# Kernel optimization log

Measured on AMD Instinct MI355X. Metric: run time of the kernel, lower is better.

The kernel has to match this reference:

```python
import jax, jax.numpy as jnp
import numpy as np

B, S, D, H, E, K = 2, 1024, 1024, 2048, 8, 2


def setup_inputs() -> dict:
    key = jax.random.key(0)
    k1, k2, k3, k4 = jax.random.split(key, 4)
    x = jax.random.normal(k1, (B, S, D), dtype=jnp.float32)
    # router initialized to zeros in the module; use small random weights so
    # top-k routing is non-degenerate for a correctness baseline
    router_w = 0.02 * jax.random.normal(k2, (E, D), dtype=jnp.float32)
    router_b = jnp.zeros((E,), dtype=jnp.float32)
    w12 = 0.02 * jax.random.normal(k3, (E, D, 2 * H), dtype=jnp.float32)
    w3 = 0.02 * jax.random.normal(k4, (E, H, D), dtype=jnp.float32)
    return {"x": x, "router_w": router_w, "router_b": router_b, "w12": w12, "w3": w3}


def reference(x, router_w, router_b, w12, w3):
    # Router (eval mode: no jitter noise)
    logits = jnp.einsum("bsd,ed->bse", x, router_w) + router_b      # [B,S,E]
    scores = jax.nn.sigmoid(logits)
    top_vals, top_idx = jax.lax.top_k(scores, K)                     # [B,S,K]
    rweights = top_vals / (jnp.sum(top_vals, axis=-1, keepdims=True) + 1e-6)
    # per-expert combine weight: sum over top-k slots where idx == e
    onehot = jax.nn.one_hot(top_idx, E, dtype=x.dtype)               # [B,S,K,E]
    combine = jnp.einsum("bsk,bske->bse", rweights, onehot)          # [B,S,E]
    # Dense per-expert SwiGLU over all tokens (matches naive module math)
    h12 = jnp.einsum("bsd,edh->ebsh", x, w12)                        # [E,B,S,2H]
    h1, h2 = jnp.split(h12, 2, axis=-1)
    hidden = jax.nn.silu(h1) * h2                                    # [E,B,S,H]
    expert_out = jnp.einsum("ebsh,ehd->ebsd", hidden, w3)            # [E,B,S,D]
    out = jnp.einsum("ebsd,bse->bsd", expert_out, combine)           # [B,S,D]
    aux_loss = 0.01 * jnp.mean(logits ** 2)
    return out, aux_loss
```

## Files before the change

### kernel.cpp

```cpp
#include <hip/hip_runtime.h>
#include <math.h>
#include <stdint.h>

#define B_ 2
#define S_ 1024
#define D_ 1024
#define H_ 2048
#define E_ 8
#define TOK_ (B_*S_)
#define N1_ (2*H_)
#define PAIRS_ (TOK_*2)
#define MAXTILES_ 40

typedef float f32x4 __attribute__((ext_vector_type(4)));
typedef short short8 __attribute__((ext_vector_type(8)));

__device__ __forceinline__ unsigned short f2bf(float f) {
  unsigned int u = __float_as_uint(f);
  u += 0x7fffu + ((u >> 16) & 1u);
  return (unsigned short)(u >> 16);
}

__global__ __launch_bounds__(256) void transpose_f32_to_bf16(
    const float* __restrict__ src, unsigned short* __restrict__ dst, int R, int C)
{
  __shared__ float tile[64][65];
  const int e = blockIdx.z;
  const float* s = src + (size_t)e * R * C;
  unsigned short* d = dst + (size_t)e * R * C;
  const int c0 = blockIdx.x * 64, r0 = blockIdx.y * 64;
  const int tx = threadIdx.x & 63;
  const int ty = threadIdx.x >> 6;
#pragma unroll
  for (int i = 0; i < 16; ++i) {
    int r = ty + i * 4;
    tile[r][tx] = s[(size_t)(r0 + r) * C + c0 + tx];
  }
  __syncthreads();
  const int rx = (threadIdx.x & 31) * 2;
  const int cy = threadIdx.x >> 5;
#pragma unroll
  for (int i = 0; i < 8; ++i) {
    int c = cy + i * 8;
    ushort2 o;
    o.x = f2bf(tile[rx][c]);
    o.y = f2bf(tile[rx + 1][c]);
    *(ushort2*)&d[(size_t)(c0 + c) * R + r0 + rx] = o;
  }
}

__global__ __launch_bounds__(256) void router_kernel(
    const float* __restrict__ x, const float* __restrict__ rw,
    const float* __restrict__ rb, int* __restrict__ counts,
    int* __restrict__ expert_of, int* __restrict__ slot_of,
    float* __restrict__ w_of, float* __restrict__ tok_ssq)
{
  const int wave = threadIdx.x >> 6, lane = threadIdx.x & 63;
  const int t = blockIdx.x * 4 + wave;
  const float4* x4 = (const float4*)(x + (size_t)t * D_);
  const float4* rw4 = (const float4*)rw;
  float acc[E_];
#pragma unroll
  for (int e = 0; e < E_; ++e) acc[e] = 0.f;
#pragma unroll
  for (int d4 = 0; d4 < D_ / 4 / 64; ++d4) {
    int idx = d4 * 64 + lane;
    float4 xv = x4[idx];
#pragma unroll
    for (int e = 0; e < E_; ++e) {
      float4 wv = rw4[e * (D_ / 4) + idx];
      acc[e] += xv.x * wv.x + xv.y * wv.y + xv.z * wv.z + xv.w * wv.w;
    }
  }
#pragma unroll
  for (int e = 0; e < E_; ++e) {
    float v = acc[e];
#pragma unroll
    for (int sh = 32; sh > 0; sh >>= 1) v += __shfl_xor(v, sh, 64);
    acc[e] = v;
  }
  if (lane == 0) {
    float logits[E_], sc[E_], ssq = 0.f;
#pragma unroll
    for (int e = 0; e < E_; ++e) {
      logits[e] = acc[e] + rb[e];
      ssq += logits[e] * logits[e];
      sc[e] = 1.f / (1.f + __expf(-logits[e]));
    }
    tok_ssq[t] = ssq;
    int i1 = 0;
#pragma unroll
    for (int e = 1; e < E_; ++e) if (sc[e] > sc[i1]) i1 = e;
    int i2 = (i1 == 0) ? 1 : 0;
#pragma unroll
    for (int e = 0; e < E_; ++e)
      if (e != i1 && e != i2 && sc[e] > sc[i2]) i2 = e;
    float v1 = sc[i1], v2 = sc[i2];
    float inv = 1.f / (v1 + v2 + 1e-6f);
    int s1 = atomicAdd(&counts[i1], 1);
    int s2 = atomicAdd(&counts[i2], 1);
    expert_of[t * 2]     = i1; slot_of[t * 2]     = s1; w_of[t * 2]     = v1 * inv;
    expert_of[t * 2 + 1] = i2; slot_of[t * 2 + 1] = s2; w_of[t * 2 + 1] = v2 * inv;
  }
}

__global__ __launch_bounds__(256) void meta_kernel(
    const int* __restrict__ counts, const float* __restrict__ tok_ssq,
    int* __restrict__ offsets, int* __restrict__ tile_e, int* __restrict__ tile_m0,
    float* __restrict__ out_aux)
{
  if (threadIdx.x == 0) {
    int o = 0, nt = 0;
    for (int e = 0; e < E_; ++e) {
      offsets[e] = o;
      for (int m0 = 0; m0 < counts[e]; m0 += 128) {
        tile_e[nt] = e; tile_m0[nt] = m0; ++nt;
      }
      o += counts[e];
    }
    for (; nt < MAXTILES_; ++nt) tile_e[nt] = -1;
  }
  __shared__ float sm[256];
  float s = 0.f;
  for (int i = threadIdx.x; i < TOK_; i += 256) s += tok_ssq[i];
  sm[threadIdx.x] = s;
  __syncthreads();
  for (int h = 128; h > 0; h >>= 1) {
    if (threadIdx.x < h) sm[threadIdx.x] += sm[threadIdx.x + h];
    __syncthreads();
  }
  if (threadIdx.x == 0) *out_aux = 0.01f * sm[0] / (float)(TOK_ * E_);
}

__global__ __launch_bounds__(256) void pack_kernel(
    const float* __restrict__ x, const int* __restrict__ expert_of,
    const int* __restrict__ slot_of, const int* __restrict__ offsets,
    unsigned short* __restrict__ px, int* __restrict__ pair_row)
{
  const int pair = blockIdx.x;
  const int t = pair >> 1;
  const int e = expert_of[pair];
  const int row = offsets[e] + slot_of[pair];
  if (threadIdx.x == 0) pair_row[pair] = row;
  const float4* xr = (const float4*)(x + (size_t)t * D_);
  ushort4* pr = (ushort4*)(px + (size_t)row * D_);
  float4 v = xr[threadIdx.x];
  ushort4 o;
  o.x = f2bf(v.x); o.y = f2bf(v.y); o.z = f2bf(v.z); o.w = f2bf(v.w);
  pr[threadIdx.x] = o;
}

__device__ __forceinline__ void stage_tile(const unsigned short* gbase, int gstride,
                                           unsigned short* sbase, int kk,
                                           int wave, int lane)
{
  const int seg = (lane & 3) ^ ((lane >> 3) & 3);
#pragma unroll
  for (int c = 0; c < 2; ++c) {
    const unsigned short* g = gbase
        + (size_t)(wave * 32 + c * 16 + (lane >> 2)) * gstride + kk + seg * 8;
    unsigned short* s = sbase + (wave * 32 + c * 16) * 32;
    __builtin_amdgcn_global_load_lds(
        (const __attribute__((address_space(1))) void*)g,
        (__attribute__((address_space(3))) void*)s, 16, 0, 0);
  }
}

__device__ __forceinline__ void stage_tile_clamped(const unsigned short* gbase, int gstride,
                                                   int row0, int rowmax,
                                                   unsigned short* sbase, int kk,
                                                   int wave, int lane)
{
  const int seg = (lane & 3) ^ ((lane >> 3) & 3);
#pragma unroll
  for (int c = 0; c < 2; ++c) {
    int r = row0 + wave * 32 + c * 16 + (lane >> 2);
    r = (r < rowmax) ? r : rowmax - 1;
    const unsigned short* g = gbase + (size_t)r * gstride + kk + seg * 8;
    unsigned short* s = sbase + (wave * 32 + c * 16) * 32;
    __builtin_amdgcn_global_load_lds(
        (const __attribute__((address_space(1))) void*)g,
        (__attribute__((address_space(3))) void*)s, 16, 0, 0);
  }
}

__device__ __forceinline__ short8 read_frag(const unsigned short* smem, int row, int lk) {
  const int s = lk ^ ((row >> 1) & 3);
  return *(const short8*)&smem[row * 32 + s * 8];
}

__global__ __launch_bounds__(256, 2) void gemm1_kernel(
    const unsigned short* __restrict__ px, const unsigned short* __restrict__ w12t,
    unsigned short* __restrict__ hid, const int* __restrict__ counts,
    const int* __restrict__ offsets, const int* __restrict__ tile_e,
    const int* __restrict__ tile_m0)
{
  const int ti = blockIdx.y, nt = blockIdx.x;
  const int e = tile_e[ti];
  if (e < 0) return;
  const int m0 = tile_m0[ti];
  const int cnt = counts[e];
  const int off = offsets[e];
  const int tid = threadIdx.x;
  const int wave = tid >> 6, lane = tid & 63;
  const int wm = wave >> 1, wn = wave & 1;
  const int lr = lane & 15, lk = lane >> 4;

  __shared__ __align__(16) unsigned short As[128 * 32];
  __shared__ __align__(16) unsigned short B1s[128 * 32];
  __shared__ __align__(16) unsigned short B2s[128 * 32];

  f32x4 zero = {0.f, 0.f, 0.f, 0.f};
  f32x4 acc1[4][4], acc2[4][4];
#pragma unroll
  for (int mi = 0; mi < 4; ++mi)
#pragma unroll
    for (int ni = 0; ni < 4; ++ni) { acc1[mi][ni] = zero; acc2[mi][ni] = zero; }

  const unsigned short* B1base = w12t + ((size_t)e * N1_ + nt * 128) * D_;
  const unsigned short* B2base = w12t + ((size_t)e * N1_ + H_ + nt * 128) * D_;

  for (int kk = 0; kk < D_; kk += 32) {
    stage_tile_clamped(px, D_, off + m0, PAIRS_, As, kk, wave, lane);
    stage_tile(B1base, D_, B1s, kk, wave, lane);
    stage_tile(B2base, D_, B2s, kk, wave, lane);
    __syncthreads();
    short8 a[4], b1[4], b2[4];
#pragma unroll
    for (int i = 0; i < 4; ++i) {
      a[i]  = read_frag(As,  wm * 64 + i * 16 + lr, lk);
      b1[i] = read_frag(B1s, wn * 64 + i * 16 + lr, lk);
      b2[i] = read_frag(B2s, wn * 64 + i * 16 + lr, lk);
    }
#pragma unroll
    for (int mi = 0; mi < 4; ++mi)
#pragma unroll
      for (int ni = 0; ni < 4; ++ni) {
        acc1[mi][ni] = __builtin_amdgcn_mfma_f32_16x16x32_bf16(a[mi], b1[ni], acc1[mi][ni], 0, 0, 0);
        acc2[mi][ni] = __builtin_amdgcn_mfma_f32_16x16x32_bf16(a[mi], b2[ni], acc2[mi][ni], 0, 0, 0);
      }
    __syncthreads();
  }

#pragma unroll
  for (int mi = 0; mi < 4; ++mi)
#pragma unroll
    for (int r = 0; r < 4; ++r) {
      int row_local = m0 + wm * 64 + mi * 16 + lk * 4 + r;
      if (row_local < cnt) {
#pragma unroll
        for (int ni = 0; ni < 4; ++ni) {
          int col = nt * 128 + wn * 64 + ni * 16 + lr;
          float v1 = acc1[mi][ni][r];
          float v2 = acc2[mi][ni][r];
          float hval = (v1 / (1.f + __expf(-v1))) * v2;
          hid[(size_t)(off + row_local) * H_ + col] = f2bf(hval);
        }
      }
    }
}

__global__ __launch_bounds__(256, 4) void gemm2_kernel(
    const unsigned short* __restrict__ hid, const unsigned short* __restrict__ w3t,
    const int* __restrict__ counts, const int* __restrict__ offsets,
    const int* __restrict__ tile_e, const int* __restrict__ tile_m0,
    float* __restrict__ ybuf)
{
  const int ti = blockIdx.y, nt = blockIdx.x, ks = blockIdx.z;
  const int e = tile_e[ti];
  if (e < 0) return;
  const int m0 = tile_m0[ti];
  const int cnt = counts[e];
  const int off = offsets[e];
  const int tid = threadIdx.x;
  const int wave = tid >> 6, lane = tid & 63;
  const int wm = wave >> 1, wn = wave & 1;
  const int lr = lane & 15, lk = lane >> 4;

  __shared__ __align__(16) unsigned short As[128 * 32];
  __shared__ __align__(16) unsigned short Bs[128 * 32];

  f32x4 zero = {0.f, 0.f, 0.f, 0.f};
  f32x4 acc[4][4];
#pragma unroll
  for (int mi = 0; mi < 4; ++mi)
#pragma unroll
    for (int ni = 0; ni < 4; ++ni) acc[mi][ni] = zero;

  const unsigned short* Bbase = w3t + ((size_t)e * D_ + nt * 128) * H_;
  float* yb = ybuf + (size_t)ks * PAIRS_ * D_;

  const int k0 = ks * (H_ / 2), k1 = k0 + (H_ / 2);
  for (int kk = k0; kk < k1; kk += 32) {
    stage_tile_clamped(hid, H_, off + m0, PAIRS_, As, kk, wave, lane);
    stage_tile(Bbase, H_, Bs, kk, wave, lane);
    __syncthreads();
    short8 a[4], b[4];
#pragma unroll
    for (int i = 0; i < 4; ++i) {
      a[i] = read_frag(As, wm * 64 + i * 16 + lr, lk);
      b[i] = read_frag(Bs, wn * 64 + i * 16 + lr, lk);
    }
#pragma unroll
    for (int mi = 0; mi < 4; ++mi)
#pragma unroll
      for (int ni = 0; ni < 4; ++ni)
        acc[mi][ni] = __builtin_amdgcn_mfma_f32_16x16x32_bf16(a[mi], b[ni], acc[mi][ni], 0, 0, 0);
    __syncthreads();
  }

#pragma unroll
  for (int mi = 0; mi < 4; ++mi)
#pragma unroll
    for (int r = 0; r < 4; ++r) {
      int row_local = m0 + wm * 64 + mi * 16 + lk * 4 + r;
      if (row_local < cnt) {
        int g = off + row_local;
#pragma unroll
        for (int ni = 0; ni < 4; ++ni) {
          int col = nt * 128 + wn * 64 + ni * 16 + lr;
          yb[(size_t)g * D_ + col] = acc[mi][ni][r];
        }
      }
    }
}

__global__ __launch_bounds__(256) void combine_kernel(
    const float* __restrict__ ybuf, const int* __restrict__ pair_row,
    const float* __restrict__ w_of, float* __restrict__ out)
{
  const int t = blockIdx.x;
  const int r0 = pair_row[t * 2], r1 = pair_row[t * 2 + 1];
  const float w0 = w_of[t * 2], w1 = w_of[t * 2 + 1];
  const float4* y0 = (const float4*)(ybuf);
  const float4* y1 = (const float4*)(ybuf + (size_t)PAIRS_ * D_);
  const int i = threadIdx.x;
  float4 a0 = y0[(size_t)r0 * (D_ / 4) + i];
  float4 b0 = y1[(size_t)r0 * (D_ / 4) + i];
  float4 a1 = y0[(size_t)r1 * (D_ / 4) + i];
  float4 b1 = y1[(size_t)r1 * (D_ / 4) + i];
  float4 o;
  o.x = w0 * (a0.x + b0.x) + w1 * (a1.x + b1.x);
  o.y = w0 * (a0.y + b0.y) + w1 * (a1.y + b1.y);
  o.z = w0 * (a0.z + b0.z) + w1 * (a1.z + b1.z);
  o.w = w0 * (a0.w + b0.w) + w1 * (a1.w + b1.w);
  ((float4*)out)[(size_t)t * (D_ / 4) + i] = o;
}

extern "C" void kernel_launch(void* const* d_in, const int* in_sizes, int n_in,
                              void* d_out, int out_size, void* d_ws, size_t ws_size,
                              hipStream_t stream)
{
  const float* x   = (const float*)d_in[0];
  const float* rw  = (const float*)d_in[1];
  const float* rb  = (const float*)d_in[2];
  const float* w12 = (const float*)d_in[3];
  const float* w3  = (const float*)d_in[4];
  float* out = (float*)d_out;

  char* wsb = (char*)d_ws;
  int*   counts    = (int*)(wsb + 0);
  int*   offsets   = (int*)(wsb + 64);
  int*   tile_e    = (int*)(wsb + 128);
  int*   tile_m0   = (int*)(wsb + 384);
  int*   expert_of = (int*)(wsb + 1024);
  int*   slot_of   = (int*)(wsb + 1024 + 16384);
  float* w_of      = (float*)(wsb + 1024 + 2 * 16384);
  int*   pair_row  = (int*)(wsb + 1024 + 3 * 16384);
  float* tok_ssq   = (float*)(wsb + 1024 + 4 * 16384);
  unsigned short* px   = (unsigned short*)(wsb + (128 << 10));
  unsigned short* hid  = (unsigned short*)(wsb + (128 << 10) + ((size_t)8  << 20));
  unsigned short* w12t = (unsigned short*)(wsb + (128 << 10) + ((size_t)24 << 20));
  unsigned short* w3t  = (unsigned short*)(wsb + (128 << 10) + ((size_t)88 << 20));
  float*          ybuf = (float*)(wsb + (128 << 10) + ((size_t)120 << 20));

  hipMemsetAsync(counts, 0, E_ * sizeof(int), stream);

  transpose_f32_to_bf16<<<dim3(N1_ / 64, D_ / 64, E_), 256, 0, stream>>>(w12, w12t, D_, N1_);
  transpose_f32_to_bf16<<<dim3(D_ / 64, H_ / 64, E_), 256, 0, stream>>>(w3, w3t, H_, D_);
  router_kernel<<<TOK_ / 4, 256, 0, stream>>>(x, rw, rb, counts, expert_of, slot_of, w_of, tok_ssq);
  meta_kernel<<<1, 256, 0, stream>>>(counts, tok_ssq, offsets, tile_e, tile_m0, out + (size_t)TOK_ * D_);
  pack_kernel<<<PAIRS_, 256, 0, stream>>>(x, expert_of, slot_of, offsets, px, pair_row);
  gemm1_kernel<<<dim3(16, MAXTILES_), 256, 0, stream>>>(px, w12t, hid, counts, offsets, tile_e, tile_m0);
  gemm2_kernel<<<dim3(8, MAXTILES_, 2), 256, 0, stream>>>(hid, w3t, counts, offsets, tile_e, tile_m0, ybuf);
  combine_kernel<<<TOK_, 256, 0, stream>>>(ybuf, pair_row, w_of, out);
}
```

Baseline: 431.0 us.

## Deepen GEMM K-tile to 64, store partial sums in bf16, vectorize weight transpose

Both grouped GEMMs now stage 64-wide K slices per iteration with a new 8-segment XOR swizzle, which halves the number of barriers and loop iterations per tile but doubles LDS use per block. The split-K partial output buffer is stored as bf16 instead of fp32, cutting the write and read traffic between gemm2 and combine at the cost of extra rounding error. The weight transpose/convert kernel is changed to float4 loads and ushort4 stores to reduce memory instruction count.

```diff
diff --git a/kernel.cpp b/kernel.cpp
--- a/kernel.cpp
+++ b/kernel.cpp
@@ -20,6 +20,9 @@
   u += 0x7fffu + ((u >> 16) & 1u);
   return (unsigned short)(u >> 16);
 }
+__device__ __forceinline__ float bf2f(unsigned short u) {
+  return __uint_as_float(((unsigned int)u) << 16);
+}
 
 __global__ __launch_bounds__(256) void transpose_f32_to_bf16(
     const float* __restrict__ src, unsigned short* __restrict__ dst, int R, int C)
@@ -29,23 +32,29 @@
   const float* s = src + (size_t)e * R * C;
   unsigned short* d = dst + (size_t)e * R * C;
   const int c0 = blockIdx.x * 64, r0 = blockIdx.y * 64;
-  const int tx = threadIdx.x & 63;
-  const int ty = threadIdx.x >> 6;
-#pragma unroll
-  for (int i = 0; i < 16; ++i) {
-    int r = ty + i * 4;
-    tile[r][tx] = s[(size_t)(r0 + r) * C + c0 + tx];
+  const int lrow = threadIdx.x >> 4;
+  const int lc4  = threadIdx.x & 15;
+#pragma unroll
+  for (int i = 0; i < 4; ++i) {
+    int r = lrow + i * 16;
+    float4 v = *(const float4*)&s[(size_t)(r0 + r) * C + c0 + lc4 * 4];
+    tile[r][lc4 * 4 + 0] = v.x;
+    tile[r][lc4 * 4 + 1] = v.y;
+    tile[r][lc4 * 4 + 2] = v.z;
+    tile[r][lc4 * 4 + 3] = v.w;
   }
   __syncthreads();
-  const int rx = (threadIdx.x & 31) * 2;
-  const int cy = threadIdx.x >> 5;
-#pragma unroll
-  for (int i = 0; i < 8; ++i) {
-    int c = cy + i * 8;
-    ushort2 o;
-    o.x = f2bf(tile[rx][c]);
+  const int rx = (threadIdx.x & 15) * 4;
+  const int cy = threadIdx.x >> 4;
+#pragma unroll
+  for (int i = 0; i < 4; ++i) {
+    int c = cy + i * 16;
+    ushort4 o;
+    o.x = f2bf(tile[rx + 0][c]);
     o.y = f2bf(tile[rx + 1][c]);
-    *(ushort2*)&d[(size_t)(c0 + c) * R + r0 + rx] = o;
+    o.z = f2bf(tile[rx + 2][c]);
+    o.w = f2bf(tile[rx + 3][c]);
+    *(ushort4*)&d[(size_t)(c0 + c) * R + r0 + rx] = o;
   }
 }
 
@@ -150,43 +159,46 @@
   pr[threadIdx.x] = o;
 }
 
-__device__ __forceinline__ void stage_tile(const unsigned short* gbase, int gstride,
-                                           unsigned short* sbase, int kk,
-                                           int wave, int lane)
-{
-  const int seg = (lane & 3) ^ ((lane >> 3) & 3);
-#pragma unroll
-  for (int c = 0; c < 2; ++c) {
-    const unsigned short* g = gbase
-        + (size_t)(wave * 32 + c * 16 + (lane >> 2)) * gstride + kk + seg * 8;
-    unsigned short* s = sbase + (wave * 32 + c * 16) * 32;
+__device__ __forceinline__ void stage64(const unsigned short* gbase, int gstride,
+                                        unsigned short* sbase, int kk,
+                                        int wave, int lane)
+{
+  const int rw = lane >> 3;
+  const int seg = (lane & 7) ^ rw;
+#pragma unroll
+  for (int c = 0; c < 4; ++c) {
+    int row = wave * 8 + c * 32 + rw;
+    const unsigned short* g = gbase + (size_t)row * gstride + kk + seg * 8;
+    unsigned short* s = sbase + (size_t)(wave * 8 + c * 32) * 64;
     __builtin_amdgcn_global_load_lds(
         (const __attribute__((address_space(1))) void*)g,
         (__attribute__((address_space(3))) void*)s, 16, 0, 0);
   }
 }
 
-__device__ __forceinline__ void stage_tile_clamped(const unsigned short* gbase, int gstride,
-                                                   int row0, int rowmax,
-                                                   unsigned short* sbase, int kk,
-                                                   int wave, int lane)
-{
-  const int seg = (lane & 3) ^ ((lane >> 3) & 3);
-#pragma unroll
-  for (int c = 0; c < 2; ++c) {
-    int r = row0 + wave * 32 + c * 16 + (lane >> 2);
-    r = (r < rowmax) ? r : rowmax - 1;
-    const unsigned short* g = gbase + (size_t)r * gstride + kk + seg * 8;
-    unsigned short* s = sbase + (wave * 32 + c * 16) * 32;
+__device__ __forceinline__ void stage64_clamped(const unsigned short* gbase, int gstride,
+                                                int row0, int rowmax,
+                                                unsigned short* sbase, int kk,
+                                                int wave, int lane)
+{
+  const int rw = lane >> 3;
+  const int seg = (lane & 7) ^ rw;
+#pragma unroll
+  for (int c = 0; c < 4; ++c) {
+    int row = row0 + wave * 8 + c * 32 + rw;
+    row = (row < rowmax) ? row : rowmax - 1;
+    const unsigned short* g = gbase + (size_t)row * gstride + kk + seg * 8;
+    unsigned short* s = sbase + (size_t)(wave * 8 + c * 32) * 64;
     __builtin_amdgcn_global_load_lds(
         (const __attribute__((address_space(1))) void*)g,
         (__attribute__((address_space(3))) void*)s, 16, 0, 0);
   }
 }
 
-__device__ __forceinline__ short8 read_frag(const unsigned short* smem, int row, int lk) {
-  const int s = lk ^ ((row >> 1) & 3);
-  return *(const short8*)&smem[row * 32 + s * 8];
+__device__ __forceinline__ short8 read_frag64(const unsigned short* smem, int row,
+                                              int j, int lk) {
+  const int s = (j * 4 + lk) ^ (row & 7);
+  return *(const short8*)&smem[row * 64 + s * 8];
 }
 
 __global__ __launch_bounds__(256, 2) void gemm1_kernel(
@@ -206,9 +218,9 @@
   const int wm = wave >> 1, wn = wave & 1;
   const int lr = lane & 15, lk = lane >> 4;
 
-  __shared__ __align__(16) unsigned short As[128 * 32];
-  __shared__ __align__(16) unsigned short B1s[128 * 32];
-  __shared__ __align__(16) unsigned short B2s[128 * 32];
+  __shared__ __align__(16) unsigned short As[128 * 64];
+  __shared__ __align__(16) unsigned short B1s[128 * 64];
+  __shared__ __align__(16) unsigned short B2s[128 * 64];
 
   f32x4 zero = {0.f, 0.f, 0.f, 0.f};
   f32x4 acc1[4][4], acc2[4][4];
@@ -220,25 +232,28 @@
   const unsigned short* B1base = w12t + ((size_t)e * N1_ + nt * 128) * D_;
   const unsigned short* B2base = w12t + ((size_t)e * N1_ + H_ + nt * 128) * D_;
 
-  for (int kk = 0; kk < D_; kk += 32) {
-    stage_tile_clamped(px, D_, off + m0, PAIRS_, As, kk, wave, lane);
-    stage_tile(B1base, D_, B1s, kk, wave, lane);
-    stage_tile(B2base, D_, B2s, kk, wave, lane);
+  for (int kk = 0; kk < D_; kk += 64) {
+    stage64_clamped(px, D_, off + m0, PAIRS_, As, kk, wave, lane);
+    stage64(B1base, D_, B1s, kk, wave, lane);
+    stage64(B2base, D_, B2s, kk, wave, lane);
     __syncthreads();
-    short8 a[4], b1[4], b2[4];
-#pragma unroll
-    for (int i = 0; i < 4; ++i) {
-      a[i]  = read_frag(As,  wm * 64 + i * 16 + lr, lk);
-      b1[i] = read_frag(B1s, wn * 64 + i * 16 + lr, lk);
-      b2[i] = read_frag(B2s, wn * 64 + i * 16 + lr, lk);
-    }
-#pragma unroll
-    for (int mi = 0; mi < 4; ++mi)
-#pragma unroll
-      for (int ni = 0; ni < 4; ++ni) {
-        acc1[mi][ni] = __builtin_amdgcn_mfma_f32_16x16x32_bf16(a[mi], b1[ni], acc1[mi][ni], 0, 0, 0);
-        acc2[mi][ni] = __builtin_amdgcn_mfma_f32_16x16x32_bf16(a[mi], b2[ni], acc2[mi][ni], 0, 0, 0);
+#pragma unroll
+    for (int j = 0; j < 2; ++j) {
+      short8 a[4], b1[4], b2[4];
+#pragma unroll
+      for (int i = 0; i < 4; ++i) {
+        a[i]  = read_frag64(As,  wm * 64 + i * 16 + lr, j, lk);
+        b1[i] = read_frag64(B1s, wn * 64 + i * 16 + lr, j, lk);
+        b2[i] = read_frag64(B2s, wn * 64 + i * 16 + lr, j, lk);
       }
+#pragma unroll
+      for (int mi = 0; mi < 4; ++mi)
+#pragma unroll
+        for (int ni = 0; ni < 4; ++ni) {
+          acc1[mi][ni] = __builtin_amdgcn_mfma_f32_16x16x32_bf16(a[mi], b1[ni], acc1[mi][ni], 0, 0, 0);
+          acc2[mi][ni] = __builtin_amdgcn_mfma_f32_16x16x32_bf16(a[mi], b2[ni], acc2[mi][ni], 0, 0, 0);
+        }
+    }
     __syncthreads();
   }
 
@@ -264,7 +279,7 @@
     const unsigned short* __restrict__ hid, const unsigned short* __restrict__ w3t,
     const int* __restrict__ counts, const int* __restrict__ offsets,
     const int* __restrict__ tile_e, const int* __restrict__ tile_m0,
-    float* __restrict__ ybuf)
+    unsigned short* __restrict__ ybuf)
 {
   const int ti = blockIdx.y, nt = blockIdx.x, ks = blockIdx.z;
   const int e = tile_e[ti];
@@ -277,8 +292,8 @@
   const int wm = wave >> 1, wn = wave & 1;
   const int lr = lane & 15, lk = lane >> 4;
 
-  __shared__ __align__(16) unsigned short As[128 * 32];
-  __shared__ __align__(16) unsigned short Bs[128 * 32];
+  __shared__ __align__(16) unsigned short As[128 * 64];
+  __shared__ __align__(16) unsigned short Bs[128 * 64];
 
   f32x4 zero = {0.f, 0.f, 0.f, 0.f};
   f32x4 acc[4][4];
@@ -288,24 +303,27 @@
     for (int ni = 0; ni < 4; ++ni) acc[mi][ni] = zero;
 
   const unsigned short* Bbase = w3t + ((size_t)e * D_ + nt * 128) * H_;
-  float* yb = ybuf + (size_t)ks * PAIRS_ * D_;
+  unsigned short* yb = ybuf + (size_t)ks * PAIRS_ * D_;
 
   const int k0 = ks * (H_ / 2), k1 = k0 + (H_ / 2);
-  for (int kk = k0; kk < k1; kk += 32) {
-    stage_tile_clamped(hid, H_, off + m0, PAIRS_, As, kk, wave, lane);
-    stage_tile(Bbase, H_, Bs, kk, wave, lane);
+  for (int kk = k0; kk < k1; kk += 64) {
+    stage64_clamped(hid, H_, off + m0, PAIRS_, As, kk, wave, lane);
+    stage64(Bbase, H_, Bs, kk, wave, lane);
     __syncthreads();
-    short8 a[4], b[4];
-#pragma unroll
-    for (int i = 0; i < 4; ++i) {
-      a[i] = read_frag(As, wm * 64 + i * 16 + lr, lk);
-      b[i] = read_frag(Bs, wn * 64 + i * 16 + lr, lk);
-    }
-#pragma unroll
-    for (int mi = 0; mi < 4; ++mi)
-#pragma unroll
-      for (int ni = 0; ni < 4; ++ni)
-        acc[mi][ni] = __builtin_amdgcn_mfma_f32_16x16x32_bf16(a[mi], b[ni], acc[mi][ni], 0, 0, 0);
+#pragma unroll
+    for (int j = 0; j < 2; ++j) {
+      short8 a[4], b[4];
+#pragma unroll
+      for (int i = 0; i < 4; ++i) {
+        a[i] = read_frag64(As, wm * 64 + i * 16 + lr, j, lk);
+        b[i] = read_frag64(Bs, wn * 64 + i * 16 + lr, j, lk);
+      }
+#pragma unroll
+      for (int mi = 0; mi < 4; ++mi)
+#pragma unroll
+        for (int ni = 0; ni < 4; ++ni)
+          acc[mi][ni] = __builtin_amdgcn_mfma_f32_16x16x32_bf16(a[mi], b[ni], acc[mi][ni], 0, 0, 0);
+    }
     __syncthreads();
   }
 
@@ -319,31 +337,30 @@
 #pragma unroll
         for (int ni = 0; ni < 4; ++ni) {
           int col = nt * 128 + wn * 64 + ni * 16 + lr;
-          yb[(size_t)g * D_ + col] = acc[mi][ni][r];
+          yb[(size_t)g * D_ + col] = f2bf(acc[mi][ni][r]);
         }
       }
     }
 }
 
 __global__ __launch_bounds__(256) void combine_kernel(
-    const float* __restrict__ ybuf, const int* __restrict__ pair_row,
+    const unsigned short* __restrict__ ybuf, const int* __restrict__ pair_row,
     const float* __restrict__ w_of, float* __restrict__ out)
 {
   const int t = blockIdx.x;
   const int r0 = pair_row[t * 2], r1 = pair_row[t * 2 + 1];
   const float w0 = w_of[t * 2], w1 = w_of[t * 2 + 1];
-  const float4* y0 = (const float4*)(ybuf);
-  const float4* y1 = (const float4*)(ybuf + (size_t)PAIRS_ * D_);
+  const unsigned short* y1p = ybuf + (size_t)PAIRS_ * D_;
   const int i = threadIdx.x;
-  float4 a0 = y0[(size_t)r0 * (D_ / 4) + i];
-  float4 b0 = y1[(size_t)r0 * (D_ / 4) + i];
-  float4 a1 = y0[(size_t)r1 * (D_ / 4) + i];
-  float4 b1 = y1[(size_t)r1 * (D_ / 4) + i];
+  ushort4 a0 = *(const ushort4*)&ybuf[(size_t)r0 * D_ + i * 4];
+  ushort4 b0 = *(const ushort4*)&y1p [(size_t)r0 * D_ + i * 4];
+  ushort4 a1 = *(const ushort4*)&ybuf[(size_t)r1 * D_ + i * 4];
+  ushort4 b1 = *(const ushort4*)&y1p [(size_t)r1 * D_ + i * 4];
   float4 o;
-  o.x = w0 * (a0.x + b0.x) + w1 * (a1.x + b1.x);
-  o.y = w0 * (a0.y + b0.y) + w1 * (a1.y + b1.y);
-  o.z = w0 * (a0.z + b0.z) + w1 * (a1.z + b1.z);
-  o.w = w0 * (a0.w + b0.w) + w1 * (a1.w + b1.w);
+  o.x = w0 * (bf2f(a0.x) + bf2f(b0.x)) + w1 * (bf2f(a1.x) + bf2f(b1.x));
+  o.y = w0 * (bf2f(a0.y) + bf2f(b0.y)) + w1 * (bf2f(a1.y) + bf2f(b1.y));
+  o.z = w0 * (bf2f(a0.z) + bf2f(b0.z)) + w1 * (bf2f(a1.z) + bf2f(b1.z));
+  o.w = w0 * (bf2f(a0.w) + bf2f(b0.w)) + w1 * (bf2f(a1.w) + bf2f(b1.w));
   ((float4*)out)[(size_t)t * (D_ / 4) + i] = o;
 }
 
@@ -372,7 +389,7 @@
   unsigned short* hid  = (unsigned short*)(wsb + (128 << 10) + ((size_t)8  << 20));
   unsigned short* w12t = (unsigned short*)(wsb + (128 << 10) + ((size_t)24 << 20));
   unsigned short* w3t  = (unsigned short*)(wsb + (128 << 10) + ((size_t)88 << 20));
-  float*          ybuf = (float*)(wsb + (128 << 10) + ((size_t)120 << 20));
+  unsigned short* ybuf = (unsigned short*)(wsb + (128 << 10) + ((size_t)120 << 20));
 
   hipMemsetAsync(counts, 0, E_ * sizeof(int), stream);
 
```

Result: faster. 417.1 us (-3.2%).
